# Kernel optimization log

Hardware: AMD Instinct MI355X
Metric: run time of the kernel (lower is better)

## Reference

```python
import jax, jax.numpy as jnp
import numpy as np

ATTENTION_HEAD = 16
EXPANSION_LENGTH = 300
TEXT_EMBEDDING_DIM = 768
LN_EPS = 1e-3  # keras LayerNormalization default epsilon


def setup_inputs() -> dict:
    key = jax.random.key(0)
    ks = jax.random.split(key, 8)
    B, L, D = 8, 2048, TEXT_EMBEDDING_DIM
    H = ATTENTION_HEAD
    E = EXPANSION_LENGTH
    dh = D // H
    glorot = lambda k, shape, fan_in, fan_out: jax.random.uniform(
        k, shape, jnp.float32,
        -jnp.sqrt(6.0 / (fan_in + fan_out)), jnp.sqrt(6.0 / (fan_in + fan_out)))
    return {
        "q": jax.random.normal(ks[0], (B, 1, L, D), jnp.float32),
        "k": jax.random.normal(ks[1], (B, 1, L, D), jnp.float32),
        "v": jax.random.normal(ks[2], (B, 1, L, D), jnp.float32),
        "Wq": glorot(ks[3], (D, D), D, D),
        "bq": jnp.zeros((D,), jnp.float32),
        "Wv": glorot(ks[4], (D, D), D, D),
        "bv": jnp.zeros((D,), jnp.float32),
        "memory": glorot(ks[5], (E, H, dh), E, dh),
        "gamma": jnp.ones((D,), jnp.float32),
        "beta": jnp.zeros((D,), jnp.float32),
    }


def reference(q, k, v, Wq, bq, Wv, bv, memory, gamma, beta):
    B, _, L, D = q.shape
    H = ATTENTION_HEAD
    dh = D // H
    # Dense projections (v is unused by the original module)
    Q_ = q @ Wq + bq                      # (B,1,L,D)
    V_ = k @ Wv + bv                      # (B,1,L,D)
    Q = Q_.reshape(B, L, H, dh)
    V = V_.reshape(B, L, H, dh)
    # memory-query scores, ReLU instead of softmax
    eij = jax.nn.relu(jnp.einsum('ehd,blhd->belh', memory, Q))  # (B,E,L,H)
    out1 = jnp.einsum('belh,blhd->behd', eij, V)                # (B,E,H,dh)
    out2 = jnp.einsum('behd,belh->blhd', out1, eij)             # (B,L,H,dh)
    x = out2.reshape(B, 1, L, D)
    mean = jnp.mean(x, axis=-1, keepdims=True)
    var = jnp.var(x, axis=-1, keepdims=True)
    return (x - mean) * jax.lax.rsqrt(var + LN_EPS) * gamma + beta
```

## Files before the change

### kernel.cpp

```cpp
#include <hip/hip_runtime.h>
#include <hip/hip_bf16.h>
#include <stdint.h>

#define B_   8
#define L_   2048
#define D_   768
#define H_   16
#define DH   48
#define E_   300
#define EP   320
#define KP   64
#define ACH  4
#define N1T  (128 * DH * EP)
#define NT_  24

typedef __bf16 bf16;
typedef __bf16 bf16x8 __attribute__((ext_vector_type(8)));
typedef __bf16 bf16x4 __attribute__((ext_vector_type(4)));
typedef float  f32x4  __attribute__((ext_vector_type(4)));

typedef const __attribute__((address_space(1))) uint32_t guint;
typedef __attribute__((address_space(3))) uint32_t luint;

__device__ __forceinline__ f32x4 mfma16(bf16x8 a, bf16x8 b, f32x4 c) {
  return __builtin_amdgcn_mfma_f32_16x16x32_bf16(a, b, c, 0, 0, 0);
}

__global__ __launch_bounds__(256) void k_wt(const float* __restrict__ Wq,
                                            const float* __restrict__ Wv,
                                            bf16* __restrict__ WqT,
                                            bf16* __restrict__ WvT) {
  int idx = blockIdx.x * 256 + threadIdx.x;
  int n = idx / D_, k = idx % D_;
  const float* W = blockIdx.y ? Wv : Wq;
  bf16* WT = blockIdx.y ? WvT : WqT;
  WT[n * D_ + k] = (bf16)W[k * D_ + n];
}

__global__ __launch_bounds__(256) void k_mem(const float* __restrict__ M,
                                             bf16* __restrict__ MP) {
  int idx = blockIdx.x * 256 + threadIdx.x;
  int h = idx / (EP * KP);
  int r = idx % (EP * KP);
  int e = r / KP, d = r % KP;
  float v = (e < E_ && d < DH) ? M[(e * H_ + h) * DH + d] : 0.f;
  MP[idx] = (bf16)v;
}

__global__ __launch_bounds__(512, 4) void k_gemm(
    const float* __restrict__ A0, const float* __restrict__ A1,
    const bf16* __restrict__ WT0, const bf16* __restrict__ WT1,
    const float* __restrict__ b0, const float* __restrict__ b1,
    bf16* __restrict__ outQ, bf16* __restrict__ outVT) {
  __shared__ bf16 As[2][128 * 32];
  __shared__ bf16 Bs[2][256 * 32];
  const int tid = threadIdx.x, lane = tid & 63, w = tid >> 6;
  const int wr = w >> 2, wc = w & 3;
  const int lr = lane & 15, lq = lane >> 4;
  const int bid = blockIdx.x;
  const int j = (bid & 7) * 48 + (bid >> 3);
  const int n0 = (j % 3) * 256, m0 = (j / 3) * 128;
  const int mode = blockIdx.y;
  const float* A = mode ? A1 : A0;
  const bf16* WT = mode ? WT1 : WT0;
  const float* bias = mode ? b1 : b0;

  const int arow = tid >> 2, ac8 = tid & 3;
  const int aslot = ac8 ^ ((arow >> 1) & 3);
  const float* aSrc = A + (size_t)(m0 + arow) * D_ + ac8 * 8;

  f32x4 acc[4][4] = {};

  auto stageB = [&](int buf, int k0) {
#pragma unroll
    for (int t = 0; t < 2; ++t) {
      int idx = tid + t * 512;
      int brow = idx >> 2, bt = idx & 3;
      int bc8 = bt ^ ((brow >> 1) & 3);
      const bf16* src = WT + (size_t)(n0 + brow) * D_ + k0 + bc8 * 8;
      __builtin_amdgcn_global_load_lds((guint*)src,
                                       (luint*)&Bs[buf][(t * 512 + w * 64) * 8], 16, 0, 0);
    }
  };

  float4 f0 = *(const float4*)(aSrc);
  float4 f1 = *(const float4*)(aSrc + 4);
  stageB(0, 0);

  for (int t = 0; t < NT_; ++t) {
    const int cur = t & 1;
    {
      bf16x8 v;
      v[0] = (bf16)f0.x; v[1] = (bf16)f0.y; v[2] = (bf16)f0.z; v[3] = (bf16)f0.w;
      v[4] = (bf16)f1.x; v[5] = (bf16)f1.y; v[6] = (bf16)f1.z; v[7] = (bf16)f1.w;
      *(bf16x8*)&As[cur][arow * 32 + aslot * 8] = v;
    }
    __syncthreads();
    if (t + 1 < NT_) {
      const float* s = aSrc + (t + 1) * 32;
      f0 = *(const float4*)s;
      f1 = *(const float4*)(s + 4);
      stageB(cur ^ 1, (t + 1) * 32);
    }
    bf16x8 af[4], bfr[4];
#pragma unroll
    for (int mi = 0; mi < 4; ++mi) {
      int row = wr * 64 + mi * 16 + lr;
      af[mi] = *(const bf16x8*)&As[cur][row * 32 + (lq ^ ((row >> 1) & 3)) * 8];
    }
#pragma unroll
    for (int ni = 0; ni < 4; ++ni) {
      int row = wc * 64 + ni * 16 + lr;
      bfr[ni] = *(const bf16x8*)&Bs[cur][row * 32 + (lq ^ ((row >> 1) & 3)) * 8];
    }
#pragma unroll
    for (int mi = 0; mi < 4; ++mi)
#pragma unroll
      for (int ni = 0; ni < 4; ++ni)
        acc[mi][ni] = mfma16(af[mi], bfr[ni], acc[mi][ni]);
  }

  float bs[4];
#pragma unroll
  for (int ni = 0; ni < 4; ++ni) bs[ni] = bias[n0 + wc * 64 + ni * 16 + lr];

  if (mode == 0) {
#pragma unroll
    for (int mi = 0; mi < 4; ++mi)
#pragma unroll
      for (int ni = 0; ni < 4; ++ni) {
        int m = m0 + wr * 64 + mi * 16 + lq * 4;
        int n = n0 + wc * 64 + ni * 16 + lr;
#pragma unroll
        for (int r = 0; r < 4; ++r)
          outQ[(size_t)(m + r) * D_ + n] = (bf16)(acc[mi][ni][r] + bs[ni]);
      }
  } else {
#pragma unroll
    for (int mi = 0; mi < 4; ++mi)
#pragma unroll
      for (int ni = 0; ni < 4; ++ni) {
        int mb = m0 + wr * 64 + mi * 16 + lq * 4;
        int n = n0 + wc * 64 + ni * 16 + lr;
        int bhd = (mb >> 11) * H_ + n / DH;
        int d = n % DH;
        int l = mb & (L_ - 1);
        bf16x4 v;
#pragma unroll
        for (int r = 0; r < 4; ++r) v[r] = (bf16)(acc[mi][ni][r] + bs[ni]);
        *(bf16x4*)&outVT[((size_t)bhd * DH + d) * L_ + l] = v;
      }
  }
}

__global__ __launch_bounds__(256) void k_phaseA(
    const bf16* __restrict__ Qb, const bf16* __restrict__ VT,
    const bf16* __restrict__ MP, float* __restrict__ O1P) {
  __shared__ bf16 Qs[2][32 * 88];
  __shared__ bf16 Vs[2][48 * 40];
  __shared__ bf16 Ss[EP * 40];
  const int tid = threadIdx.x, lane = tid & 63, w = tid >> 6;
  const int lr = lane & 15, lq = lane >> 4;
  const int bh = blockIdx.y, b = bh >> 4, h = bh & 15;
  const int lbase = blockIdx.x * (L_ / ACH);

  bf16x8 mf[5][2];
#pragma unroll
  for (int mi = 0; mi < 5; ++mi)
#pragma unroll
    for (int kh = 0; kh < 2; ++kh)
      mf[mi][kh] = *(const bf16x8*)&MP[(size_t)(h * EP + w * 80 + mi * 16 + lr) * KP + kh * 32 + lq * 8];

  if (tid < 128) {
    int buf = tid >> 6, t = tid & 63;
    uint4 z = {0, 0, 0, 0};
    *(uint4*)&Qs[buf][(t >> 1) * 88 + 48 + (t & 1) * 8] = z;
  }

  auto loadQ = [&](int idx, int l0) {
    return *(const bf16x8*)&Qb[(size_t)(b * L_ + l0 + idx / 6) * D_ + h * DH + (idx % 6) * 8];
  };
  auto loadV = [&](int j, int l0) {
    return *(const bf16x8*)&VT[((size_t)bh * DH + (j >> 2)) * L_ + l0 + (j & 3) * 8];
  };

  bf16x8 rA, rB;
  {
    int l0 = lbase;
    rA = (tid < 192) ? loadQ(tid, l0) : loadV(tid - 192, l0);
    if (tid < 128) rB = loadV(tid + 64, l0);
  }

  f32x4 acc[5][3] = {};

  for (int it = 0; it < L_ / ACH / 32; ++it) {
    const int cur = it & 1;
    if (tid < 192) *(bf16x8*)&Qs[cur][(tid / 6) * 88 + (tid % 6) * 8] = rA;
    else           *(bf16x8*)&Vs[cur][((tid - 192) >> 2) * 40 + ((tid - 192) & 3) * 8] = rA;
    if (tid < 128) *(bf16x8*)&Vs[cur][((tid + 64) >> 2) * 40 + ((tid + 64) & 3) * 8] = rB;
    __syncthreads();
    if (it + 1 < L_ / ACH / 32) {
      int l0 = lbase + (it + 1) * 32;
      rA = (tid < 192) ? loadQ(tid, l0) : loadV(tid - 192, l0);
      if (tid < 128) rB = loadV(tid + 64, l0);
    }
    bf16x8 qf[2][2];
#pragma unroll
    for (int ni = 0; ni < 2; ++ni)
#pragma unroll
      for (int kh = 0; kh < 2; ++kh)
        qf[ni][kh] = *(const bf16x8*)&Qs[cur][(ni * 16 + lr) * 88 + kh * 32 + lq * 8];
#pragma unroll
    for (int mi = 0; mi < 5; ++mi)
#pragma unroll
      for (int ni = 0; ni < 2; ++ni) {
        f32x4 s = {0.f, 0.f, 0.f, 0.f};
        s = mfma16(mf[mi][0], qf[ni][0], s);
        s = mfma16(mf[mi][1], qf[ni][1], s);
#pragma unroll
        for (int r = 0; r < 4; ++r)
          Ss[(w * 80 + mi * 16 + lq * 4 + r) * 40 + ni * 16 + lr] =
              (bf16)(s[r] > 0.f ? s[r] : 0.f);
      }
    bf16x8 sf[5], vf[3];
#pragma unroll
    for (int mi = 0; mi < 5; ++mi)
      sf[mi] = *(const bf16x8*)&Ss[(w * 80 + mi * 16 + lr) * 40 + lq * 8];
#pragma unroll
    for (int ni = 0; ni < 3; ++ni)
      vf[ni] = *(const bf16x8*)&Vs[cur][(ni * 16 + lr) * 40 + lq * 8];
#pragma unroll
    for (int mi = 0; mi < 5; ++mi)
#pragma unroll
      for (int ni = 0; ni < 3; ++ni)
        acc[mi][ni] = mfma16(sf[mi], vf[ni], acc[mi][ni]);
  }
  float* dst = O1P + (size_t)(blockIdx.x * 128 + bh) * DH * EP;
#pragma unroll
  for (int mi = 0; mi < 5; ++mi)
#pragma unroll
    for (int ni = 0; ni < 3; ++ni) {
      int e = w * 80 + mi * 16 + lq * 4;
      int d = ni * 16 + lr;
#pragma unroll
      for (int r = 0; r < 4; ++r)
        dst[(size_t)d * EP + e + r] = acc[mi][ni][r];
    }
}

__global__ __launch_bounds__(256) void k_red(const float* __restrict__ O1P,
                                             bf16* __restrict__ O1T) {
  int idx = blockIdx.x * 256 + threadIdx.x;
  if (idx >= N1T) return;
  float s = O1P[idx];
#pragma unroll
  for (int c = 1; c < ACH; ++c) s += O1P[(size_t)c * N1T + idx];
  O1T[idx] = (bf16)s;
}

__global__ __launch_bounds__(256, 4) void k_phaseB(
    const bf16* __restrict__ Qb, const bf16* __restrict__ MP,
    const bf16* __restrict__ O1T, bf16* __restrict__ X) {
  __shared__ bf16 Qs[64 * 88];
  __shared__ bf16 STs[64 * 76];
  __shared__ bf16 O1s[2][48 * 76];
  const int tid = threadIdx.x, lane = tid & 63, w = tid >> 6;
  const int lr = lane & 15, lq = lane >> 4;
  const int bh = blockIdx.y, b = bh >> 4, h = bh & 15;
  const int l0 = blockIdx.x * 64;

  bf16x8 mfB[5][2];
#pragma unroll
  for (int c = 0; c < 5; ++c)
#pragma unroll
    for (int kh = 0; kh < 2; ++kh)
      mfB[c][kh] = *(const bf16x8*)&MP[(size_t)(h * EP + c * 64 + w * 16 + lr) * KP + kh * 32 + lq * 8];

  for (int idx = tid; idx < 512; idx += 256) {
    if (idx < 384) {
      int row = idx / 6, c = idx % 6;
      *(bf16x8*)&Qs[row * 88 + c * 8] =
          *(const bf16x8*)&Qb[(size_t)(b * L_ + l0 + row) * D_ + h * DH + c * 8];
    } else {
      int j = idx - 384;
      uint4 z = {0, 0, 0, 0};
      *(uint4*)&Qs[(j >> 1) * 88 + 48 + (j & 1) * 8] = z;
    }
  }
  for (int idx = tid; idx < 384; idx += 256)
    *(bf16x8*)&O1s[0][(idx >> 3) * 76 + (idx & 7) * 8] =
        *(const bf16x8*)&O1T[((size_t)bh * DH + (idx >> 3)) * EP + (idx & 7) * 8];
  __syncthreads();

  f32x4 acc[3] = {};
#pragma unroll
  for (int c = 0; c < 5; ++c) {
    bf16x8 r0, r1;
    if (c < 4) {
      r0 = *(const bf16x8*)&O1T[((size_t)bh * DH + (tid >> 3)) * EP + (c + 1) * 64 + (tid & 7) * 8];
      if (tid < 128) {
        int i2 = tid + 256;
        r1 = *(const bf16x8*)&O1T[((size_t)bh * DH + (i2 >> 3)) * EP + (c + 1) * 64 + (i2 & 7) * 8];
      }
    }
#pragma unroll
    for (int mi = 0; mi < 4; ++mi) {
      bf16x8 qa0 = *(const bf16x8*)&Qs[(mi * 16 + lr) * 88 + lq * 8];
      bf16x8 qa1 = *(const bf16x8*)&Qs[(mi * 16 + lr) * 88 + 32 + lq * 8];
      f32x4 s = {0.f, 0.f, 0.f, 0.f};
      s = mfma16(qa0, mfB[c][0], s);
      s = mfma16(qa1, mfB[c][1], s);
#pragma unroll
      for (int r = 0; r < 4; ++r)
        STs[(mi * 16 + lq * 4 + r) * 76 + w * 16 + lr] =
            (bf16)(s[r] > 0.f ? s[r] : 0.f);
    }
    __syncthreads();
#pragma unroll
    for (int ks = 0; ks < 2; ++ks) {
      bf16x8 sf = *(const bf16x8*)&STs[(w * 16 + lr) * 76 + ks * 32 + lq * 8];
#pragma unroll
      for (int ni = 0; ni < 3; ++ni) {
        bf16x8 of = *(const bf16x8*)&O1s[c & 1][(ni * 16 + lr) * 76 + ks * 32 + lq * 8];
        acc[ni] = mfma16(sf, of, acc[ni]);
      }
    }
    if (c < 4) {
      *(bf16x8*)&O1s[(c + 1) & 1][(tid >> 3) * 76 + (tid & 7) * 8] = r0;
      if (tid < 128) {
        int i2 = tid + 256;
        *(bf16x8*)&O1s[(c + 1) & 1][(i2 >> 3) * 76 + (i2 & 7) * 8] = r1;
      }
    }
    __syncthreads();
  }
#pragma unroll
  for (int ni = 0; ni < 3; ++ni)
#pragma unroll
    for (int r = 0; r < 4; ++r)
      X[(size_t)(b * L_ + l0 + w * 16 + lq * 4 + r) * D_ + h * DH + ni * 16 + lr] =
          (bf16)acc[ni][r];
}

__global__ __launch_bounds__(256) void k_ln(
    const bf16* __restrict__ X, const float* __restrict__ gamma,
    const float* __restrict__ beta, float* __restrict__ out) {
  const int lane = threadIdx.x & 63;
  const int row = blockIdx.x * 4 + (threadIdx.x >> 6);
  const bf16* x = X + (size_t)row * D_;
  float v[12];
#pragma unroll
  for (int c = 0; c < 3; ++c) {
    bf16x4 ch = *(const bf16x4*)(x + lane * 12 + c * 4);
#pragma unroll
    for (int j = 0; j < 4; ++j) v[c * 4 + j] = (float)ch[j];
  }
  float s = 0.f, q = 0.f;
#pragma unroll
  for (int j = 0; j < 12; ++j) { s += v[j]; q += v[j] * v[j]; }
#pragma unroll
  for (int off = 32; off > 0; off >>= 1) {
    s += __shfl_xor(s, off);
    q += __shfl_xor(q, off);
  }
  float mean = s * (1.f / 768.f);
  float var = q * (1.f / 768.f) - mean * mean;
  float inv = rsqrtf(var + 1e-3f);
  float* o = out + (size_t)row * D_;
#pragma unroll
  for (int c = 0; c < 3; ++c) {
    float4 g = *(const float4*)(gamma + lane * 12 + c * 4);
    float4 bt = *(const float4*)(beta + lane * 12 + c * 4);
    float4 r;
    r.x = (v[c * 4 + 0] - mean) * inv * g.x + bt.x;
    r.y = (v[c * 4 + 1] - mean) * inv * g.y + bt.y;
    r.z = (v[c * 4 + 2] - mean) * inv * g.z + bt.z;
    r.w = (v[c * 4 + 3] - mean) * inv * g.w + bt.w;
    *(float4*)(o + lane * 12 + c * 4) = r;
  }
}

extern "C" void kernel_launch(void* const* d_in, const int* in_sizes, int n_in,
                              void* d_out, int out_size, void* d_ws, size_t ws_size,
                              hipStream_t stream) {
  (void)in_sizes; (void)n_in; (void)out_size; (void)ws_size;
  const float* q_in = (const float*)d_in[0];
  const float* k_in = (const float*)d_in[1];
  const float* Wq   = (const float*)d_in[3];
  const float* bq   = (const float*)d_in[4];
  const float* Wv   = (const float*)d_in[5];
  const float* bv   = (const float*)d_in[6];
  const float* mem  = (const float*)d_in[7];
  const float* gam  = (const float*)d_in[8];
  const float* bet  = (const float*)d_in[9];
  float* out = (float*)d_out;

  char* ws = (char*)d_ws;
  size_t off = 0;
  auto alloc = [&](size_t bytes) {
    char* p = ws + off;
    off += (bytes + 255) & ~(size_t)255;
    return p;
  };
  bf16*  WqT = (bf16*)alloc((size_t)D_ * D_ * 2);
  bf16*  WvT = (bf16*)alloc((size_t)D_ * D_ * 2);
  bf16*  MP  = (bf16*)alloc((size_t)H_ * EP * KP * 2);
  bf16*  Qb  = (bf16*)alloc((size_t)B_ * L_ * D_ * 2);
  bf16*  VT  = (bf16*)alloc((size_t)B_ * H_ * DH * L_ * 2);
  bf16*  O1T = (bf16*)alloc((size_t)N1T * 2);
  const size_t o1pBytes = (size_t)ACH * N1T * 4;
  const size_t xbBytes  = (size_t)B_ * L_ * D_ * 2;
  char*  big = alloc(xbBytes > o1pBytes ? xbBytes : o1pBytes);
  float* O1P = (float*)big;
  bf16*  Xb  = (bf16*)big;

  k_wt<<<dim3((D_ * D_) / 256, 2), 256, 0, stream>>>(Wq, Wv, WqT, WvT);
  k_mem<<<(H_ * EP * KP) / 256, 256, 0, stream>>>(mem, MP);
  k_gemm<<<dim3(384, 2), 512, 0, stream>>>(q_in, k_in, WqT, WvT, bq, bv, Qb, VT);
  k_phaseA<<<dim3(ACH, B_ * H_), 256, 0, stream>>>(Qb, VT, MP, O1P);
  k_red<<<(N1T + 255) / 256, 256, 0, stream>>>(O1P, O1T);
  k_phaseB<<<dim3(L_ / 64, B_ * H_), 256, 0, stream>>>(Qb, MP, O1T, Xb);
  k_ln<<<(B_ * L_) / 4, 256, 0, stream>>>(Xb, gam, bet, out);
}
```

Before: 178.2 us.

## Triple-buffer projection GEMM staging with deeper prefetch of A and B tiles

The Q/V projection GEMM moves from double to triple LDS buffering, keeping A-tile register prefetch two iterations ahead and B tiles (via global_load_lds) two stages ahead. The loop is unrolled by three with explicit waitcnt and barrier placement plus a sched_barrier, so memory latency is hidden behind MFMA work. The launch-bounds occupancy hint drops from 4 to 2 because shared memory per block grows to about 72 KB. The risk is lower occupancy and more register pressure from the three A prefetch sets.

```diff
diff --git a/kernel.cpp b/kernel.cpp
--- a/kernel.cpp
+++ b/kernel.cpp
@@ -47,13 +47,13 @@
   MP[idx] = (bf16)v;
 }
 
-__global__ __launch_bounds__(512, 4) void k_gemm(
+__global__ __launch_bounds__(512, 2) void k_gemm(
     const float* __restrict__ A0, const float* __restrict__ A1,
     const bf16* __restrict__ WT0, const bf16* __restrict__ WT1,
     const float* __restrict__ b0, const float* __restrict__ b1,
     bf16* __restrict__ outQ, bf16* __restrict__ outVT) {
-  __shared__ bf16 As[2][128 * 32];
-  __shared__ bf16 Bs[2][256 * 32];
+  __shared__ bf16 As[3][128 * 32];
+  __shared__ bf16 Bs[3][256 * 32];
   const int tid = threadIdx.x, lane = tid & 63, w = tid >> 6;
   const int wr = w >> 2, wc = w & 3;
   const int lr = lane & 15, lq = lane >> 4;
@@ -65,11 +65,9 @@
   const bf16* WT = mode ? WT1 : WT0;
   const float* bias = mode ? b1 : b0;
 
-  const int arow = tid >> 2, ac8 = tid & 3;
-  const int aslot = ac8 ^ ((arow >> 1) & 3);
-  const float* aSrc = A + (size_t)(m0 + arow) * D_ + ac8 * 8;
-
-  f32x4 acc[4][4] = {};
+  const int arow = tid >> 2, ac = tid & 3;
+  const int aslot = ac ^ ((arow >> 1) & 3);
+  const float* aSrc = A + (size_t)(m0 + arow) * D_ + ac * 8;
 
   auto stageB = [&](int buf, int k0) {
 #pragma unroll
@@ -79,46 +77,70 @@
       int bc8 = bt ^ ((brow >> 1) & 3);
       const bf16* src = WT + (size_t)(n0 + brow) * D_ + k0 + bc8 * 8;
       __builtin_amdgcn_global_load_lds((guint*)src,
-                                       (luint*)&Bs[buf][(t * 512 + w * 64) * 8], 16, 0, 0);
+          (luint*)&Bs[buf][(t * 512 + w * 64) * 8], 16, 0, 0);
     }
   };
 
-  float4 f0 = *(const float4*)(aSrc);
-  float4 f1 = *(const float4*)(aSrc + 4);
+  f32x4 acc[4][4] = {};
+  float4 aR0[2], aR1[2], aR2[2];
+
+#define LOADA(SET, T)                                        \
+  { const float* s_ = aSrc + (T) * 32;                       \
+    SET[0] = *(const float4*)s_;                             \
+    SET[1] = *(const float4*)(s_ + 4); }
+#define COMMITA(SET, BUF)                                    \
+  { bf16x8 v_;                                               \
+    v_[0]=(bf16)SET[0].x; v_[1]=(bf16)SET[0].y;              \
+    v_[2]=(bf16)SET[0].z; v_[3]=(bf16)SET[0].w;              \
+    v_[4]=(bf16)SET[1].x; v_[5]=(bf16)SET[1].y;              \
+    v_[6]=(bf16)SET[1].z; v_[7]=(bf16)SET[1].w;              \
+    *(bf16x8*)&As[BUF][arow * 32 + aslot * 8] = v_; }
+
   stageB(0, 0);
-
-  for (int t = 0; t < NT_; ++t) {
-    const int cur = t & 1;
-    {
-      bf16x8 v;
-      v[0] = (bf16)f0.x; v[1] = (bf16)f0.y; v[2] = (bf16)f0.z; v[3] = (bf16)f0.w;
-      v[4] = (bf16)f1.x; v[5] = (bf16)f1.y; v[6] = (bf16)f1.z; v[7] = (bf16)f1.w;
-      *(bf16x8*)&As[cur][arow * 32 + aslot * 8] = v;
-    }
-    __syncthreads();
-    if (t + 1 < NT_) {
-      const float* s = aSrc + (t + 1) * 32;
-      f0 = *(const float4*)s;
-      f1 = *(const float4*)(s + 4);
-      stageB(cur ^ 1, (t + 1) * 32);
-    }
-    bf16x8 af[4], bfr[4];
-#pragma unroll
-    for (int mi = 0; mi < 4; ++mi) {
-      int row = wr * 64 + mi * 16 + lr;
-      af[mi] = *(const bf16x8*)&As[cur][row * 32 + (lq ^ ((row >> 1) & 3)) * 8];
-    }
-#pragma unroll
-    for (int ni = 0; ni < 4; ++ni) {
-      int row = wc * 64 + ni * 16 + lr;
-      bfr[ni] = *(const bf16x8*)&Bs[cur][row * 32 + (lq ^ ((row >> 1) & 3)) * 8];
-    }
-#pragma unroll
-    for (int mi = 0; mi < 4; ++mi)
-#pragma unroll
-      for (int ni = 0; ni < 4; ++ni)
-        acc[mi][ni] = mfma16(af[mi], bfr[ni], acc[mi][ni]);
-  }
+  LOADA(aR0, 0);
+  COMMITA(aR0, 0);
+  stageB(1, 32);
+  LOADA(aR1, 1);
+  LOADA(aR2, 2);
+
+#define GBODY(TT, K, CSET, LSET)                                         \
+  {                                                                      \
+    const int t_ = (TT) + (K);                                           \
+    if (t_ + 1 < NT_) { COMMITA(CSET, ((K) + 1) % 3); }                  \
+    else { asm volatile("s_waitcnt vmcnt(0)" ::: "memory"); }            \
+    asm volatile("s_waitcnt lgkmcnt(0)" ::: "memory");                   \
+    __builtin_amdgcn_s_barrier();                                        \
+    __builtin_amdgcn_sched_barrier(0);                                   \
+    if (t_ + 2 < NT_) stageB(((K) + 2) % 3, (t_ + 2) * 32);              \
+    if (t_ + 3 < NT_) LOADA(LSET, t_ + 3);                               \
+    bf16x8 af[4], bfr[4];                                                \
+    _Pragma("unroll")                                                    \
+    for (int mi = 0; mi < 4; ++mi) {                                     \
+      int row = wr * 64 + mi * 16 + lr;                                  \
+      af[mi] = *(const bf16x8*)&As[(K) % 3]                              \
+                   [row * 32 + ((lq ^ ((row >> 1) & 3)) * 8)];           \
+    }                                                                    \
+    _Pragma("unroll")                                                    \
+    for (int ni = 0; ni < 4; ++ni) {                                     \
+      int row = wc * 64 + ni * 16 + lr;                                  \
+      bfr[ni] = *(const bf16x8*)&Bs[(K) % 3]                             \
+                   [row * 32 + ((lq ^ ((row >> 1) & 3)) * 8)];           \
+    }                                                                    \
+    _Pragma("unroll")                                                    \
+    for (int mi = 0; mi < 4; ++mi)                                       \
+      _Pragma("unroll")                                                  \
+      for (int ni = 0; ni < 4; ++ni)                                     \
+        acc[mi][ni] = mfma16(af[mi], bfr[ni], acc[mi][ni]);              \
+  }
+
+  for (int tt = 0; tt < NT_; tt += 3) {
+    GBODY(tt, 0, aR1, aR0);
+    GBODY(tt, 1, aR2, aR1);
+    GBODY(tt, 2, aR0, aR2);
+  }
+#undef GBODY
+#undef LOADA
+#undef COMMITA
 
   float bs[4];
 #pragma unroll
```

Measured after the change: 179.3 us. No clear change (+0.6%).
